# Kernel tuning notes

Hardware: AMD Instinct MI355X
Metric: run time of the kernel (lower is better)

## Reference

```python
import jax, jax.numpy as jnp
import numpy as np

N_TOKENS = 4096
HIDDEN = 1024
N_EXPERTS = 8
TOP_K = 2
EXPANDED = 2048


def setup_inputs() -> dict:
    key = jax.random.key(0)
    ks = jax.random.split(key, 4)
    tokens = jax.random.normal(ks[0], (N_TOKENS, HIDDEN), dtype=jnp.float32)
    router_w = jax.random.normal(ks[1], (N_EXPERTS, HIDDEN), dtype=jnp.float32) * (1.0 / np.sqrt(HIDDEN))
    router_b = jnp.zeros((N_EXPERTS,), dtype=jnp.float32)
    w1 = jax.random.normal(ks[2], (N_EXPERTS, HIDDEN, EXPANDED), dtype=jnp.float32) * (1.0 / np.sqrt(HIDDEN))
    b1 = jnp.zeros((N_EXPERTS, EXPANDED), dtype=jnp.float32)
    w2 = jax.random.normal(ks[3], (N_EXPERTS, EXPANDED, HIDDEN), dtype=jnp.float32) * (1.0 / np.sqrt(EXPANDED))
    b2 = jnp.zeros((N_EXPERTS, HIDDEN), dtype=jnp.float32)
    return {"tokens": tokens, "router_w": router_w, "router_b": router_b,
            "w1": w1, "b1": b1, "w2": w2, "b2": b2}


def reference(tokens, router_w, router_b, w1, b1, w2, b2):
    # Router: logits [N, E], top-k scores -> softmax over the k selected experts.
    logits = tokens @ router_w.T + router_b
    top_scores, expert_ids = jax.lax.top_k(logits, TOP_K)      # [N, K]
    probs = jax.nn.softmax(top_scores, axis=-1)                # [N, K]

    # Instead of gathering full per-token weight matrices (as the torch code does),
    # run each expert's dense MLP over all tokens and combine with the per-token
    # routing weight for that expert. Identical math: each token's contribution is
    # sum_k probs[n,k] * MLP_{expert_ids[n,k]}(tokens[n]).
    out = jnp.zeros_like(tokens)
    for e in range(N_EXPERTS):
        h = jax.nn.gelu(tokens @ w1[e] + b1[e], approximate=False)  # [N, EXPANDED]
        o = h @ w2[e] + b2[e]                                       # [N, HIDDEN]
        # Combined routing weight for expert e (top_k indices are distinct).
        gate = jnp.sum(jnp.where(expert_ids == e, probs, 0.0), axis=-1)  # [N]
        out = out + gate[:, None] * o
    return out
```

## Files before the change

### kernel.cpp

```cpp
#include <hip/hip_runtime.h>
#include <hip/hip_bf16.h>

typedef unsigned short u16;
typedef __attribute__((ext_vector_type(8))) short short8;
typedef __attribute__((ext_vector_type(4))) float f32x4;

#define N_TOKENS 4096
#define HIDDEN   1024
#define N_EXP    8
#define EXPAND   2048

#define TOKB_OFF  0ull
#define W1T_OFF   8388608ull
#define OBUF_OFF  8388608ull
#define W2T_OFF   41943040ull
#define H_OFF     75497472ull
#define RLT_OFF   109051904ull
#define RLG_OFF   109084672ull
#define CNT_OFF   109117440ull
#define E01_OFF   109117472ull
#define GATE_OFF  109183008ull
#define ROWS2_OFF 109215776ull

__device__ __forceinline__ u16 f2bf(float f) {
  union { float f; unsigned u; } v; v.f = f;
  unsigned r = v.u + 0x7fffu + ((v.u >> 16) & 1u);
  return (u16)(r >> 16);
}

__device__ __forceinline__ float bf2f(u16 b) {
  union { unsigned u; float f; } v; v.u = ((unsigned)b) << 16;
  return v.f;
}

__device__ __forceinline__ void glds16(const void* g, void* l) {
  __builtin_amdgcn_global_load_lds(
      (const __attribute__((address_space(1))) void*)g,
      (__attribute__((address_space(3))) void*)l, 16, 0, 0);
}

__device__ __forceinline__ float gelu_tanh(float x) {
  float u = x * (0.7978845608f + 0.0356774081f * x * x);
  float t = __expf(-2.0f * fabsf(u));
  float th = (1.0f - t) / (1.0f + t);
  th = (u >= 0.0f) ? th : -th;
  return 0.5f * x * (1.0f + th);
}

__global__ __launch_bounds__(256) void cvt_transpose_k(const float* __restrict__ in,
                                                       u16* __restrict__ out,
                                                       int R, int C) {
  __shared__ u16 t[64][66];
  int e = blockIdx.z;
  int c0 = blockIdx.x * 64, r0 = blockIdx.y * 64;
  const float* ip = in + (size_t)e * R * C;
  u16* op = out + (size_t)e * R * C;
  int tid = threadIdx.x;
  #pragma unroll
  for (int i = 0; i < 16; ++i) {
    int flat = i * 256 + tid;
    int row = flat >> 6, col = flat & 63;
    t[row][col] = f2bf(ip[(size_t)(r0 + row) * C + c0 + col]);
  }
  __syncthreads();
  #pragma unroll
  for (int i = 0; i < 16; ++i) {
    int flat = i * 256 + tid;
    int orow = flat >> 6, ocol = flat & 63;
    op[(size_t)(c0 + orow) * R + r0 + ocol] = t[ocol][orow];
  }
}

__global__ __launch_bounds__(256) void logits_k(const float* __restrict__ tokens,
                                                const float* __restrict__ rw,
                                                const float* __restrict__ rb,
                                                u16* __restrict__ tokb,
                                                int* __restrict__ e01,
                                                float* __restrict__ gates) {
  __shared__ float rwl[N_EXP * HIDDEN];
  int tid = threadIdx.x;
  for (int i = tid; i < N_EXP * HIDDEN / 4; i += 256)
    ((float4*)rwl)[i] = ((const float4*)rw)[i];
  __syncthreads();
  int w = tid >> 6, l = tid & 63;
  int t = blockIdx.x * 4 + w;
  const float* tp = tokens + (size_t)t * HIDDEN;
  u16* tb = tokb + (size_t)t * HIDDEN;
  float acc[8] = {0.f,0.f,0.f,0.f,0.f,0.f,0.f,0.f};
  #pragma unroll
  for (int it = 0; it < 4; ++it) {
    int k = it * 256 + l * 4;
    float4 tv = *(const float4*)&tp[k];
    ushort4 o;
    o.x = f2bf(tv.x); o.y = f2bf(tv.y); o.z = f2bf(tv.z); o.w = f2bf(tv.w);
    *(ushort4*)&tb[k] = o;
    #pragma unroll
    for (int e = 0; e < 8; ++e) {
      const float4 rv = *(const float4*)&rwl[e * HIDDEN + k];
      acc[e] += tv.x * rv.x + tv.y * rv.y + tv.z * rv.z + tv.w * rv.w;
    }
  }
  #pragma unroll
  for (int off = 32; off >= 1; off >>= 1) {
    #pragma unroll
    for (int e = 0; e < 8; ++e) acc[e] += __shfl_xor(acc[e], off);
  }
  if (l == 0) {
    float lg[8];
    #pragma unroll
    for (int e = 0; e < 8; ++e) lg[e] = acc[e] + rb[e];
    int b0 = 0; float v0 = lg[0];
    #pragma unroll
    for (int e = 1; e < 8; ++e) if (lg[e] > v0) { v0 = lg[e]; b0 = e; }
    int b1 = -1; float v1 = -3.4e38f;
    #pragma unroll
    for (int e = 0; e < 8; ++e) {
      if (e == b0) continue;
      if (lg[e] > v1) { v1 = lg[e]; b1 = e; }
    }
    float d = expf(v1 - v0);
    float p1 = d / (1.f + d);
    float p0 = 1.f - p1;
    e01[t * 2] = b0;   e01[t * 2 + 1] = b1;
    gates[t * 2] = p0; gates[t * 2 + 1] = p1;
  }
}

__global__ __launch_bounds__(1024) void order_k(const int* __restrict__ e01,
                                                const float* __restrict__ gates,
                                                int* __restrict__ cnt,
                                                int* __restrict__ rlt,
                                                float* __restrict__ rlg,
                                                int* __restrict__ rows2) {
  __shared__ int slotbuf[2 * N_TOKENS];
  __shared__ int wcnt[16][N_EXP];
  __shared__ int base_run[N_EXP];
  __shared__ int basep[N_EXP];
  int tid = threadIdx.x, w = tid >> 6, l = tid & 63;
  if (tid < N_EXP) base_run[tid] = 0;
  __syncthreads();
  unsigned long long ltmask = (1ull << l) - 1ull;
  #pragma unroll
  for (int c = 0; c < 8; ++c) {
    int i = c * 1024 + tid;
    int ei = e01[i];
    int myrank = 0;
    #pragma unroll
    for (int e = 0; e < N_EXP; ++e) {
      unsigned long long b = __ballot(ei == e);
      if (l == 0) wcnt[w][e] = __popcll(b);
      if (ei == e) myrank = __popcll(b & ltmask);
    }
    __syncthreads();
    if (tid < N_EXP) {
      int e = tid, off = base_run[e];
      #pragma unroll
      for (int ww = 0; ww < 16; ++ww) {
        int v = wcnt[ww][e]; wcnt[ww][e] = off; off += v;
      }
      base_run[e] = off;
    }
    __syncthreads();
    slotbuf[i] = wcnt[w][ei] + myrank;
    __syncthreads();
  }
  if (tid < N_EXP) cnt[tid] = base_run[tid];
  if (tid == 0) {
    int s = 0;
    for (int e = 0; e < N_EXP; ++e) { basep[e] = s; s += base_run[e]; }
  }
  __syncthreads();
  #pragma unroll
  for (int c = 0; c < 8; ++c) {
    int i = c * 1024 + tid;
    int e = e01[i];
    int row = basep[e] + slotbuf[i];
    rlt[row] = i >> 1;
    rlg[row] = gates[i];
    rows2[i] = row;
  }
}


#define VM6  asm volatile("s_waitcnt vmcnt(6)" ::: "memory")
#define VM0  asm volatile("s_waitcnt vmcnt(0)" ::: "memory")

#define STAGE(Ad, Bd, KT) {                                                      \
  _Pragma("unroll") for (int c = 0; c < 4; ++c)                                  \
    glds16(ga[c] + (size_t)(KT) * 64, &Ad[(c * 256 + threadIdx.x) * 8]);         \
  _Pragma("unroll") for (int c = 0; c < 2; ++c)                                  \
    glds16(gb[c] + (size_t)(KT) * 64, &Bd[(c * 256 + threadIdx.x) * 8]);         \
}

#define GEMM_TILE(As, Bs) {                                                      \
  _Pragma("unroll") for (int kk = 0; kk < 2; ++kk) {                             \
    short8 afr[4], bfr[2];                                                       \
    _Pragma("unroll") for (int i = 0; i < 4; ++i)                                \
      afr[i] = *(const short8*)&As[oa[kk][i]];                                   \
    _Pragma("unroll") for (int j = 0; j < 2; ++j)                                \
      bfr[j] = *(const short8*)&Bs[ob[kk][j]];                                   \
    _Pragma("unroll") for (int i = 0; i < 4; ++i)                                \
      _Pragma("unroll") for (int j = 0; j < 2; ++j)                              \
        acc[i][j] = __builtin_amdgcn_mfma_f32_16x16x32_bf16(                     \
            afr[i], bfr[j], acc[i][j], 0, 0, 0);                                 \
  }                                                                              \
}

#define FRAG_OFFSETS {                                                           \
  _Pragma("unroll") for (int kk = 0; kk < 2; ++kk) {                             \
    int cc = kk * 4 + lg;                                                        \
    _Pragma("unroll") for (int i = 0; i < 4; ++i) {                              \
      int Ra = wr * 64 + i * 16 + lr;                                            \
      oa[kk][i] = Ra * 64 + (cc ^ (Ra & 7)) * 8;                                 \
    }                                                                            \
    _Pragma("unroll") for (int j = 0; j < 2; ++j) {                              \
      int Rb = wc * 32 + j * 16 + lr;                                            \
      ob[kk][j] = Rb * 64 + (cc ^ (Rb & 7)) * 8;                                 \
    }                                                                            \
  }                                                                              \
}

#define KSTEP(Ac, Bc, As, Bs, KT, NK) {                                          \
  if ((KT) + 2 < (NK)) STAGE(As, Bs, (KT) + 2)                                   \
  GEMM_TILE(Ac, Bc)                                                              \
  if ((KT) + 2 < (NK)) { VM6; }                                                  \
  else if ((KT) + 1 < (NK)) { VM0; }                                             \
  __builtin_amdgcn_s_barrier();                                                  \
  __builtin_amdgcn_sched_barrier(0);                                             \
}

#define K3(k, NK) KSTEP(A0, B0, A2, B2, (k), NK)                                 \
                  KSTEP(A1, B1, A0, B0, (k) + 1, NK)                             \
                  KSTEP(A2, B2, A1, B1, (k) + 2, NK)

#define KPROLOGUE { STAGE(A0, B0, 0) STAGE(A1, B1, 1) VM6;                       \
  __builtin_amdgcn_s_barrier(); __builtin_amdgcn_sched_barrier(0); }

__global__ __launch_bounds__(256) void ffn1_k(const u16* __restrict__ tok,
                                              const u16* __restrict__ w1t,
                                              const float* __restrict__ b1,
                                              const int* __restrict__ rlt,
                                              const int* __restrict__ cnt,
                                              u16* __restrict__ h) {
  __shared__ __align__(16) short A0[8192];
  __shared__ __align__(16) short A1[8192];
  __shared__ __align__(16) short A2[8192];
  __shared__ __align__(16) short B0[4096];
  __shared__ __align__(16) short B1[4096];
  __shared__ __align__(16) short B2[4096];

  int tid = threadIdx.x, w = tid >> 6, l = tid & 63;
  int wr = w >> 1, wc = w & 1;
  int lr = l & 15, lg = l >> 4;
  int oa[2][4], ob[2][2];
  FRAG_OFFSETS

  int e = blockIdx.x & 7;
  int rnk = blockIdx.x >> 3;
  int estr = gridDim.x >> 3;
  int m0 = 0;
  #pragma unroll
  for (int i = 0; i < 8; ++i) { int ci = cnt[i]; if (i < e) m0 += ci; }
  int ne = cnt[e];
  int mts = (ne + 127) >> 7;
  int NT_e = mts * (EXPAND / 64);

  for (int r = rnk; r < NT_e; r += estr) {
    int mt = r >> 5, nt = r & 31;
    int m0g = m0 + mt * 128;
    int mrem = ne - mt * 128;

    const u16* ga[4]; const u16* gb[2];
    #pragma unroll
    for (int c = 0; c < 4; ++c) {
      int flat = c * 256 + tid, rih = flat >> 3;
      int ch = (flat & 7) ^ (rih & 7);
      int tokid = rlt[m0g + ((rih < mrem) ? rih : 0)];
      ga[c] = tok + (size_t)tokid * HIDDEN + ch * 8;
    }
    #pragma unroll
    for (int c = 0; c < 2; ++c) {
      int flat = c * 256 + tid, rih = flat >> 3;
      int ch = (flat & 7) ^ (rih & 7);
      int nrow = nt * 64 + rih;
      gb[c] = w1t + (size_t)e * (EXPAND * HIDDEN) + (size_t)nrow * HIDDEN + ch * 8;
    }

    f32x4 acc[4][2] = {};
    KPROLOGUE
    K3(0, 16) K3(3, 16) K3(6, 16) K3(9, 16) K3(12, 16)
    KSTEP(A0, B0, A2, B2, 15, 16)

    #pragma unroll
    for (int i = 0; i < 4; ++i) {
      #pragma unroll
      for (int rr = 0; rr < 4; ++rr) {
        int row = wr * 64 + i * 16 + lg * 4 + rr;
        if (row >= mrem) continue;
        size_t hrow = (size_t)(m0g + row) * EXPAND;
        #pragma unroll
        for (int j = 0; j < 2; ++j) {
          int col = nt * 64 + wc * 32 + j * 16 + lr;
          float x = acc[i][j][rr] + b1[e * EXPAND + col];
          h[hrow + col] = f2bf(gelu_tanh(x));
        }
      }
    }
  }
}

__global__ __launch_bounds__(256) void ffn2_k(const u16* __restrict__ h,
                                              const u16* __restrict__ w2t,
                                              const float* __restrict__ b2,
                                              const float* __restrict__ rlg,
                                              const int* __restrict__ cnt,
                                              u16* __restrict__ obuf) {
  __shared__ __align__(16) short A0[8192];
  __shared__ __align__(16) short A1[8192];
  __shared__ __align__(16) short A2[8192];
  __shared__ __align__(16) short B0[4096];
  __shared__ __align__(16) short B1[4096];
  __shared__ __align__(16) short B2[4096];

  int tid = threadIdx.x, w = tid >> 6, l = tid & 63;
  int wr = w >> 1, wc = w & 1;
  int lr = l & 15, lg = l >> 4;
  int oa[2][4], ob[2][2];
  FRAG_OFFSETS

  int e = blockIdx.x & 7;
  int rnk = blockIdx.x >> 3;
  int estr = gridDim.x >> 3;
  int m0 = 0;
  #pragma unroll
  for (int i = 0; i < 8; ++i) { int ci = cnt[i]; if (i < e) m0 += ci; }
  int ne = cnt[e];
  int mts = (ne + 127) >> 7;
  int NT_e = mts * (HIDDEN / 64);

  for (int r = rnk; r < NT_e; r += estr) {
    int mt = r >> 4, nt = r & 15;
    int m0g = m0 + mt * 128;
    int mrem = ne - mt * 128;

    const u16* ga[4]; const u16* gb[2];
    #pragma unroll
    for (int c = 0; c < 4; ++c) {
      int flat = c * 256 + tid, rih = flat >> 3;
      int ch = (flat & 7) ^ (rih & 7);
      int rowg = m0g + ((rih < mrem) ? rih : 0);
      ga[c] = h + (size_t)rowg * EXPAND + ch * 8;
    }
    #pragma unroll
    for (int c = 0; c < 2; ++c) {
      int flat = c * 256 + tid, rih = flat >> 3;
      int ch = (flat & 7) ^ (rih & 7);
      int nrow = nt * 64 + rih;
      gb[c] = w2t + (size_t)e * (HIDDEN * EXPAND) + (size_t)nrow * EXPAND + ch * 8;
    }

    f32x4 acc[4][2] = {};
    KPROLOGUE
    K3(0, 32) K3(3, 32) K3(6, 32) K3(9, 32) K3(12, 32)
    K3(15, 32) K3(18, 32) K3(21, 32) K3(24, 32) K3(27, 32)
    KSTEP(A0, B0, A2, B2, 30, 32)
    KSTEP(A1, B1, A0, B0, 31, 32)

    #pragma unroll
    for (int i = 0; i < 4; ++i) {
      #pragma unroll
      for (int rr = 0; rr < 4; ++rr) {
        int row = wr * 64 + i * 16 + lg * 4 + rr;
        if (row >= mrem) continue;
        float gate = rlg[m0g + row];
        size_t orow = (size_t)(m0g + row) * HIDDEN;
        #pragma unroll
        for (int j = 0; j < 2; ++j) {
          int col = nt * 64 + wc * 32 + j * 16 + lr;
          obuf[orow + col] = f2bf((acc[i][j][rr] + b2[e * HIDDEN + col]) * gate);
        }
      }
    }
  }
}

__global__ __launch_bounds__(256) void combine_k(const u16* __restrict__ obuf,
                                                 const int* __restrict__ rows2,
                                                 float* __restrict__ out) {
  int t = blockIdx.x, c = threadIdx.x;
  int r0 = rows2[t * 2], r1 = rows2[t * 2 + 1];
  ushort4 a = ((const ushort4*)obuf)[(size_t)r0 * 256 + c];
  ushort4 b = ((const ushort4*)obuf)[(size_t)r1 * 256 + c];
  float4 o;
  o.x = bf2f(a.x) + bf2f(b.x);
  o.y = bf2f(a.y) + bf2f(b.y);
  o.z = bf2f(a.z) + bf2f(b.z);
  o.w = bf2f(a.w) + bf2f(b.w);
  ((float4*)out)[(size_t)t * 256 + c] = o;
}

extern "C" void kernel_launch(void* const* d_in, const int* in_sizes, int n_in,
                              void* d_out, int out_size, void* d_ws, size_t ws_size,
                              hipStream_t stream) {
  const float* tokens   = (const float*)d_in[0];
  const float* router_w = (const float*)d_in[1];
  const float* router_b = (const float*)d_in[2];
  const float* w1       = (const float*)d_in[3];
  const float* b1       = (const float*)d_in[4];
  const float* w2       = (const float*)d_in[5];
  const float* b2       = (const float*)d_in[6];
  float* out = (float*)d_out;

  char* ws = (char*)d_ws;
  u16*   tokb  = (u16*)(ws + TOKB_OFF);
  u16*   w1t   = (u16*)(ws + W1T_OFF);
  u16*   obuf  = (u16*)(ws + OBUF_OFF);
  u16*   w2t   = (u16*)(ws + W2T_OFF);
  u16*   h     = (u16*)(ws + H_OFF);
  int*   rlt   = (int*)(ws + RLT_OFF);
  float* rlg   = (float*)(ws + RLG_OFF);
  int*   cnt   = (int*)(ws + CNT_OFF);
  int*   e01   = (int*)(ws + E01_OFF);
  float* gates = (float*)(ws + GATE_OFF);
  int*   rows2 = (int*)(ws + ROWS2_OFF);

  cvt_transpose_k<<<dim3(EXPAND / 64, HIDDEN / 64, N_EXP), 256, 0, stream>>>(
      w1, w1t, HIDDEN, EXPAND);
  cvt_transpose_k<<<dim3(HIDDEN / 64, EXPAND / 64, N_EXP), 256, 0, stream>>>(
      w2, w2t, EXPAND, HIDDEN);
  logits_k<<<N_TOKENS / 4, 256, 0, stream>>>(tokens, router_w, router_b, tokb, e01, gates);
  order_k<<<1, 1024, 0, stream>>>(e01, gates, cnt, rlt, rlg, rows2);
  ffn1_k<<<2048, 256, 0, stream>>>(tokb, w1t, b1, rlt, cnt, h);
  ffn2_k<<<2048, 256, 0, stream>>>(h, w2t, b2, rlg, cnt, obuf);
  combine_k<<<N_TOKENS, 256, 0, stream>>>(obuf, rows2, out);
}
```

Measured before the change: 211.3 us.

## Widen FFN GEMM tiles to 128x128 with double-buffered LDS pipeline

Both FFN GEMM kernels move from 128x64 output tiles with a three-stage hand-scheduled LDS pipeline to 128x128 tiles with a simpler two-buffer loop using __syncthreads. Each wave now holds a 4x4 MFMA accumulator grid, which doubles the arithmetic per LDS fragment load and per global B-tile fetch. The grid shrinks from 2048 to 512 blocks. The cost is fewer tiles, which can leave CUs idle when expert counts are uneven, more registers per thread, and a shallower prefetch that hides less memory latency.

```diff
diff --git a/kernel.cpp b/kernel.cpp
--- a/kernel.cpp
+++ b/kernel.cpp
@@ -182,25 +182,22 @@
 }
 
 
-#define VM6  asm volatile("s_waitcnt vmcnt(6)" ::: "memory")
-#define VM0  asm volatile("s_waitcnt vmcnt(0)" ::: "memory")
-
 #define STAGE(Ad, Bd, KT) {                                                      \
-  _Pragma("unroll") for (int c = 0; c < 4; ++c)                                  \
+  _Pragma("unroll") for (int c = 0; c < 4; ++c) {                                \
     glds16(ga[c] + (size_t)(KT) * 64, &Ad[(c * 256 + threadIdx.x) * 8]);         \
-  _Pragma("unroll") for (int c = 0; c < 2; ++c)                                  \
     glds16(gb[c] + (size_t)(KT) * 64, &Bd[(c * 256 + threadIdx.x) * 8]);         \
+  }                                                                              \
 }
 
 #define GEMM_TILE(As, Bs) {                                                      \
   _Pragma("unroll") for (int kk = 0; kk < 2; ++kk) {                             \
-    short8 afr[4], bfr[2];                                                       \
+    short8 afr[4], bfr[4];                                                       \
+    _Pragma("unroll") for (int i = 0; i < 4; ++i) {                              \
+      afr[i] = *(const short8*)&As[oa[kk][i]];                                   \
+      bfr[i] = *(const short8*)&Bs[ob[kk][i]];                                   \
+    }                                                                            \
     _Pragma("unroll") for (int i = 0; i < 4; ++i)                                \
-      afr[i] = *(const short8*)&As[oa[kk][i]];                                   \
-    _Pragma("unroll") for (int j = 0; j < 2; ++j)                                \
-      bfr[j] = *(const short8*)&Bs[ob[kk][j]];                                   \
-    _Pragma("unroll") for (int i = 0; i < 4; ++i)                                \
-      _Pragma("unroll") for (int j = 0; j < 2; ++j)                              \
+      _Pragma("unroll") for (int j = 0; j < 4; ++j)                              \
         acc[i][j] = __builtin_amdgcn_mfma_f32_16x16x32_bf16(                     \
             afr[i], bfr[j], acc[i][j], 0, 0, 0);                                 \
   }                                                                              \
@@ -212,29 +209,11 @@
     _Pragma("unroll") for (int i = 0; i < 4; ++i) {                              \
       int Ra = wr * 64 + i * 16 + lr;                                            \
       oa[kk][i] = Ra * 64 + (cc ^ (Ra & 7)) * 8;                                 \
-    }                                                                            \
-    _Pragma("unroll") for (int j = 0; j < 2; ++j) {                              \
-      int Rb = wc * 32 + j * 16 + lr;                                            \
-      ob[kk][j] = Rb * 64 + (cc ^ (Rb & 7)) * 8;                                 \
+      int Rb = wc * 64 + i * 16 + lr;                                            \
+      ob[kk][i] = Rb * 64 + (cc ^ (Rb & 7)) * 8;                                 \
     }                                                                            \
   }                                                                              \
 }
-
-#define KSTEP(Ac, Bc, As, Bs, KT, NK) {                                          \
-  if ((KT) + 2 < (NK)) STAGE(As, Bs, (KT) + 2)                                   \
-  GEMM_TILE(Ac, Bc)                                                              \
-  if ((KT) + 2 < (NK)) { VM6; }                                                  \
-  else if ((KT) + 1 < (NK)) { VM0; }                                             \
-  __builtin_amdgcn_s_barrier();                                                  \
-  __builtin_amdgcn_sched_barrier(0);                                             \
-}
-
-#define K3(k, NK) KSTEP(A0, B0, A2, B2, (k), NK)                                 \
-                  KSTEP(A1, B1, A0, B0, (k) + 1, NK)                             \
-                  KSTEP(A2, B2, A1, B1, (k) + 2, NK)
-
-#define KPROLOGUE { STAGE(A0, B0, 0) STAGE(A1, B1, 1) VM6;                       \
-  __builtin_amdgcn_s_barrier(); __builtin_amdgcn_sched_barrier(0); }
 
 __global__ __launch_bounds__(256) void ffn1_k(const u16* __restrict__ tok,
                                               const u16* __restrict__ w1t,
@@ -244,15 +223,13 @@
                                               u16* __restrict__ h) {
   __shared__ __align__(16) short A0[8192];
   __shared__ __align__(16) short A1[8192];
-  __shared__ __align__(16) short A2[8192];
-  __shared__ __align__(16) short B0[4096];
-  __shared__ __align__(16) short B1[4096];
-  __shared__ __align__(16) short B2[4096];
+  __shared__ __align__(16) short B0[8192];
+  __shared__ __align__(16) short B1[8192];
 
   int tid = threadIdx.x, w = tid >> 6, l = tid & 63;
   int wr = w >> 1, wc = w & 1;
   int lr = l & 15, lg = l >> 4;
-  int oa[2][4], ob[2][2];
+  int oa[2][4], ob[2][4];
   FRAG_OFFSETS
 
   int e = blockIdx.x & 7;
@@ -263,33 +240,36 @@
   for (int i = 0; i < 8; ++i) { int ci = cnt[i]; if (i < e) m0 += ci; }
   int ne = cnt[e];
   int mts = (ne + 127) >> 7;
-  int NT_e = mts * (EXPAND / 64);
+  int NT_e = mts * (EXPAND / 128);
 
   for (int r = rnk; r < NT_e; r += estr) {
-    int mt = r >> 5, nt = r & 31;
+    int mt = r >> 4, nt = r & 15;
     int m0g = m0 + mt * 128;
     int mrem = ne - mt * 128;
 
-    const u16* ga[4]; const u16* gb[2];
+    const u16* ga[4]; const u16* gb[4];
     #pragma unroll
     for (int c = 0; c < 4; ++c) {
       int flat = c * 256 + tid, rih = flat >> 3;
       int ch = (flat & 7) ^ (rih & 7);
       int tokid = rlt[m0g + ((rih < mrem) ? rih : 0)];
       ga[c] = tok + (size_t)tokid * HIDDEN + ch * 8;
-    }
-    #pragma unroll
-    for (int c = 0; c < 2; ++c) {
-      int flat = c * 256 + tid, rih = flat >> 3;
-      int ch = (flat & 7) ^ (rih & 7);
-      int nrow = nt * 64 + rih;
+      int nrow = nt * 128 + rih;
       gb[c] = w1t + (size_t)e * (EXPAND * HIDDEN) + (size_t)nrow * HIDDEN + ch * 8;
     }
 
-    f32x4 acc[4][2] = {};
-    KPROLOGUE
-    K3(0, 16) K3(3, 16) K3(6, 16) K3(9, 16) K3(12, 16)
-    KSTEP(A0, B0, A2, B2, 15, 16)
+    f32x4 acc[4][4] = {};
+    STAGE(A0, B0, 0)
+    __syncthreads();
+    #pragma unroll 1
+    for (int it = 0; it < 8; ++it) {
+      STAGE(A1, B1, 2 * it + 1)
+      GEMM_TILE(A0, B0)
+      __syncthreads();
+      if (it < 7) STAGE(A0, B0, 2 * it + 2)
+      GEMM_TILE(A1, B1)
+      __syncthreads();
+    }
 
     #pragma unroll
     for (int i = 0; i < 4; ++i) {
@@ -299,8 +279,8 @@
         if (row >= mrem) continue;
         size_t hrow = (size_t)(m0g + row) * EXPAND;
         #pragma unroll
-        for (int j = 0; j < 2; ++j) {
-          int col = nt * 64 + wc * 32 + j * 16 + lr;
+        for (int j = 0; j < 4; ++j) {
+          int col = nt * 128 + wc * 64 + j * 16 + lr;
           float x = acc[i][j][rr] + b1[e * EXPAND + col];
           h[hrow + col] = f2bf(gelu_tanh(x));
         }
@@ -317,15 +297,13 @@
                                               u16* __restrict__ obuf) {
   __shared__ __align__(16) short A0[8192];
   __shared__ __align__(16) short A1[8192];
-  __shared__ __align__(16) short A2[8192];
-  __shared__ __align__(16) short B0[4096];
-  __shared__ __align__(16) short B1[4096];
-  __shared__ __align__(16) short B2[4096];
+  __shared__ __align__(16) short B0[8192];
+  __shared__ __align__(16) short B1[8192];
 
   int tid = threadIdx.x, w = tid >> 6, l = tid & 63;
   int wr = w >> 1, wc = w & 1;
   int lr = l & 15, lg = l >> 4;
-  int oa[2][4], ob[2][2];
+  int oa[2][4], ob[2][4];
   FRAG_OFFSETS
 
   int e = blockIdx.x & 7;
@@ -336,35 +314,36 @@
   for (int i = 0; i < 8; ++i) { int ci = cnt[i]; if (i < e) m0 += ci; }
   int ne = cnt[e];
   int mts = (ne + 127) >> 7;
-  int NT_e = mts * (HIDDEN / 64);
+  int NT_e = mts * (HIDDEN / 128);
 
   for (int r = rnk; r < NT_e; r += estr) {
-    int mt = r >> 4, nt = r & 15;
+    int mt = r >> 3, nt = r & 7;
     int m0g = m0 + mt * 128;
     int mrem = ne - mt * 128;
 
-    const u16* ga[4]; const u16* gb[2];
+    const u16* ga[4]; const u16* gb[4];
     #pragma unroll
     for (int c = 0; c < 4; ++c) {
       int flat = c * 256 + tid, rih = flat >> 3;
       int ch = (flat & 7) ^ (rih & 7);
       int rowg = m0g + ((rih < mrem) ? rih : 0);
       ga[c] = h + (size_t)rowg * EXPAND + ch * 8;
-    }
-    #pragma unroll
-    for (int c = 0; c < 2; ++c) {
-      int flat = c * 256 + tid, rih = flat >> 3;
-      int ch = (flat & 7) ^ (rih & 7);
-      int nrow = nt * 64 + rih;
+      int nrow = nt * 128 + rih;
       gb[c] = w2t + (size_t)e * (HIDDEN * EXPAND) + (size_t)nrow * EXPAND + ch * 8;
     }
 
-    f32x4 acc[4][2] = {};
-    KPROLOGUE
-    K3(0, 32) K3(3, 32) K3(6, 32) K3(9, 32) K3(12, 32)
-    K3(15, 32) K3(18, 32) K3(21, 32) K3(24, 32) K3(27, 32)
-    KSTEP(A0, B0, A2, B2, 30, 32)
-    KSTEP(A1, B1, A0, B0, 31, 32)
+    f32x4 acc[4][4] = {};
+    STAGE(A0, B0, 0)
+    __syncthreads();
+    #pragma unroll 1
+    for (int it = 0; it < 16; ++it) {
+      STAGE(A1, B1, 2 * it + 1)
+      GEMM_TILE(A0, B0)
+      __syncthreads();
+      if (it < 15) STAGE(A0, B0, 2 * it + 2)
+      GEMM_TILE(A1, B1)
+      __syncthreads();
+    }
 
     #pragma unroll
     for (int i = 0; i < 4; ++i) {
@@ -375,8 +354,8 @@
         float gate = rlg[m0g + row];
         size_t orow = (size_t)(m0g + row) * HIDDEN;
         #pragma unroll
-        for (int j = 0; j < 2; ++j) {
-          int col = nt * 64 + wc * 32 + j * 16 + lr;
+        for (int j = 0; j < 4; ++j) {
+          int col = nt * 128 + wc * 64 + j * 16 + lr;
           obuf[orow + col] = f2bf((acc[i][j][rr] + b2[e * HIDDEN + col]) * gate);
         }
       }
@@ -430,7 +409,7 @@
       w2, w2t, EXPAND, HIDDEN);
   logits_k<<<N_TOKENS / 4, 256, 0, stream>>>(tokens, router_w, router_b, tokb, e01, gates);
   order_k<<<1, 1024, 0, stream>>>(e01, gates, cnt, rlt, rlg, rows2);
-  ffn1_k<<<2048, 256, 0, stream>>>(tokb, w1t, b1, rlt, cnt, h);
-  ffn2_k<<<2048, 256, 0, stream>>>(h, w2t, b2, rlg, cnt, obuf);
+  ffn1_k<<<512, 256, 0, stream>>>(tokb, w1t, b1, rlt, cnt, h);
+  ffn2_k<<<512, 256, 0, stream>>>(h, w2t, b2, rlg, cnt, obuf);
   combine_k<<<N_TOKENS, 256, 0, stream>>>(obuf, rows2, out);
 }
```

Result: slower. 231.7 us (+9.7%).
